# Kernel optimization log

Hardware: AMD Instinct MI355X
Metric: run time of the kernel (lower is better)

Reference implementation:

```python
import jax, jax.numpy as jnp
import numpy as np

B, N, NEMBED, E, H = 4, 256, 10000, 63, 128
D = E + 1  # feature dim after concat = 64


def _lin(key, fan_in, fan_out):
    k1, k2 = jax.random.split(key)
    bound = 1.0 / np.sqrt(fan_in)
    W = jax.random.uniform(k1, (fan_in, fan_out), jnp.float32, -bound, bound)
    b = jax.random.uniform(k2, (fan_out,), jnp.float32, -bound, bound)
    return W, b


def setup_inputs() -> dict:
    key = jax.random.key(0)
    ks = jax.random.split(key, 9)
    xcat = jax.random.randint(ks[0], (B, N), 0, NEMBED, dtype=jnp.int64)
    xfeat = jax.random.normal(ks[1], (B, N), dtype=jnp.float32)
    emb = jax.random.normal(ks[2], (NEMBED, E), dtype=jnp.float32)
    W1, b1 = _lin(ks[3], D, H)
    W2, b2 = _lin(ks[4], H, H)
    W3, b3 = _lin(ks[5], H, H)
    D1, c1 = _lin(ks[6], H, H)
    D2, c2 = _lin(ks[7], H, H)
    D3, c3 = _lin(ks[8], H, 1)
    return {"xcat": xcat, "xfeat": xfeat, "emb": emb,
            "W1": W1, "b1": b1, "W2": W2, "b2": b2, "W3": W3, "b3": b3,
            "D1": D1, "c1": c1, "D2": D2, "c2": c2, "D3": D3, "c3": c3}


def reference(xcat, xfeat, emb, W1, b1, W2, b2, W3, b3, D1, c1, D2, c2, D3, c3):
    # embed + concat scalar feature -> [B, N, D]
    x = jnp.concatenate([emb[xcat], xfeat[..., None]], axis=-1)
    # pairwise outer product over the set dim -> [B, N, N, D]
    # (original: einsum 'bid,bjd->bdij' then permute(0,2,3,1) == 'bid,bjd->bijd')
    p = jnp.einsum('bid,bjd->bijd', x, x)
    # per-pair 3-layer MLP (enc)
    h = jnp.maximum(p @ W1 + b1, 0.0)
    h = jnp.maximum(h @ W2 + b2, 0.0)
    h = h @ W3 + b3
    # relu -> mean pool over (i, j) -> relu; dropout is identity in eval
    h = jnp.maximum(h, 0.0)
    h = jnp.mean(h, axis=(1, 2))  # [B, H]
    h = jnp.maximum(h, 0.0)
    # dec MLP -> [B, 1]
    h = jnp.maximum(h @ D1 + c1, 0.0)
    h = jnp.maximum(h @ D2 + c2, 0.0)
    return h @ D3 + c3
```

## Files before the change

### kernel.cpp

```cpp
#include <hip/hip_runtime.h>
#include <hip/hip_bf16.h>


#define NB 4
#define NN 256
#define HD 128
#define TPB 257

typedef __attribute__((ext_vector_type(8))) short bf16x8;
typedef __attribute__((ext_vector_type(4))) float f32x4;

__device__ __forceinline__ unsigned rne2(float a, float b) {
    unsigned ua = __builtin_bit_cast(unsigned, a);
    unsigned ub = __builtin_bit_cast(unsigned, b);
    ua = ua + 0x7fff + ((ua >> 16) & 1);
    ub = ub + 0x7fff + ((ub >> 16) & 1);
    return (ua >> 16) | (ub & 0xffff0000u);
}

__device__ __forceinline__ short f2bf(float f) {
    unsigned u = __builtin_bit_cast(unsigned, f);
    u = (u + 0x7fff + ((u >> 16) & 1)) >> 16;
    return (short)u;
}

__device__ __forceinline__ void tri_ij(int t, int& i, int& j) {
    j = (int)((sqrtf(8.0f * (float)t + 1.0f) - 1.0f) * 0.5f);
    while (((j + 1) * (j + 2) >> 1) <= t) ++j;
    while (((j * (j + 1)) >> 1) > t) --j;
    i = t - ((j * (j + 1)) >> 1);
}

__device__ __forceinline__ void pack_w(const float* __restrict__ W, short* __restrict__ pw,
                                       int KQ, int u) {
    int l  = u & 63;
    int kq = (u >> 6) % KQ;
    int mt = (u >> 6) / KQ;
    int q = l >> 4, m = l & 15;
    int c = mt * 16 + m;
#pragma unroll
    for (int j = 0; j < 8; ++j) {
        int k = kq * 32 + q * 8 + j;
        pw[u * 8 + j] = f2bf(W[k * 128 + c]);
    }
}

__global__ void prep_kernel(const int* __restrict__ xcat,
                            const float* __restrict__ xfeat,
                            const float* __restrict__ emb,
                            const float* __restrict__ W1,
                            const float* __restrict__ W2,
                            const float* __restrict__ W3,
                            float* __restrict__ x,
                            short* __restrict__ pw1,
                            short* __restrict__ pw2,
                            short* __restrict__ pw3)
{
    int bid = blockIdx.x;
    int tid = threadIdx.x;
    if (bid < 256) {
        int f = bid * 256 + tid;
        int d = f & 63;
        int nn = f >> 6;
        float v;
        if (d < 63) v = emb[xcat[nn] * 63 + d];
        else        v = xfeat[nn];
        x[f] = v;
    } else if (bid < 260) {
        pack_w(W1, pw1, 2, (bid - 256) * 256 + tid);
    } else if (bid < 268) {
        pack_w(W2, pw2, 4, (bid - 260) * 256 + tid);
    } else {
        pack_w(W3, pw3, 4, (bid - 268) * 256 + tid);
    }
}

__global__ __launch_bounds__(256, 3) void pair_mlp(
    const float* __restrict__ x,
    const short* __restrict__ pw1, const float* __restrict__ b1,
    const short* __restrict__ pw2, const float* __restrict__ b2,
    const short* __restrict__ pw3, const float* __restrict__ b3,
    float* __restrict__ partialOut)
{
    __shared__ short smP[128 * 64];
    __shared__ short smH[128 * 128];
    __shared__ float smW[128];

    const int tid = threadIdx.x;
    const int l = tid & 63;
    const int w = __builtin_amdgcn_readfirstlane(tid >> 6);
    const int wm = w >> 1;
    const int wn = w & 1;
    const int q = l >> 4;
    const int m = l & 15;
    const int b = blockIdx.y;
    const int tbase = blockIdx.x * 128;
    const float* xb = x + (b << 14);
    char* smPc = (char*)smP;
    char* smHc = (char*)smH;

    {
        const int p = tid >> 1;
        const int half = tid & 1;
        int i, j;
        tri_ij(tbase + p, i, j);
        if (half == 0) smW[p] = (i == j) ? 1.0f : 2.0f;
        const float4* xi4 = (const float4*)(xb + (i << 6) + half * 32);
        const float4* xj4 = (const float4*)(xb + (j << 6) + half * 32);
#pragma unroll
        for (int c = 0; c < 4; ++c) {
            float4 a0 = xi4[2 * c], a1 = xi4[2 * c + 1];
            float4 u0 = xj4[2 * c], u1 = xj4[2 * c + 1];
            uint4 s;
            s.x = rne2(a0.x * u0.x, a0.y * u0.y);
            s.y = rne2(a0.z * u0.z, a0.w * u0.w);
            s.z = rne2(a1.x * u1.x, a1.y * u1.y);
            s.w = rne2(a1.z * u1.z, a1.w * u1.w);
            int chunk = half * 4 + c;
            int phys = chunk ^ (p & 7);
            *(uint4*)(smPc + p * 128 + phys * 16) = s;
        }
    }
    __syncthreads();

    f32x4 acc[4][4];

#pragma unroll
    for (int mt = 0; mt < 4; ++mt) {
        float4 bv = *(const float4*)(b1 + (wm * 4 + mt) * 16 + q * 4);
        f32x4 init = {bv.x, bv.y, bv.z, bv.w};
#pragma unroll
        for (int nt = 0; nt < 4; ++nt) acc[mt][nt] = init;
    }

#pragma unroll
    for (int kq = 0; kq < 2; ++kq) {
        bf16x8 bfr[4], afr[4];
#pragma unroll
        for (int nt = 0; nt < 4; ++nt) {
            int pair = wn * 64 + nt * 16 + m;
            int phys = (kq * 4 + q) ^ (pair & 7);
            bfr[nt] = *(const bf16x8*)(smPc + pair * 128 + phys * 16);
        }
#pragma unroll
        for (int mt = 0; mt < 4; ++mt)
            afr[mt] = *(const bf16x8*)(pw1 + ((((wm * 4 + mt) * 2 + kq) * 64 + l) << 3));
#pragma unroll
        for (int mt = 0; mt < 4; ++mt)
#pragma unroll
            for (int nt = 0; nt < 4; ++nt)
                acc[mt][nt] = __builtin_amdgcn_mfma_f32_16x16x32_bf16(afr[mt], bfr[nt], acc[mt][nt], 0, 0, 0);
    }

#pragma unroll
    for (int mt = 0; mt < 4; ++mt) {
        int mtg = wm * 4 + mt;
#pragma unroll
        for (int nt = 0; nt < 4; ++nt) {
            int pair = wn * 64 + nt * 16 + m;
            uint2 sv;
            sv.x = rne2(fmaxf(acc[mt][nt][0], 0.f), fmaxf(acc[mt][nt][1], 0.f));
            sv.y = rne2(fmaxf(acc[mt][nt][2], 0.f), fmaxf(acc[mt][nt][3], 0.f));
            int chunk = mtg * 2 + (q >> 1);
            int phys = chunk ^ (pair & 15);
            *(uint2*)(smHc + pair * 256 + phys * 16 + (q & 1) * 8) = sv;
        }
    }
    __syncthreads();

#pragma unroll
    for (int mt = 0; mt < 4; ++mt) {
        float4 bv = *(const float4*)(b2 + (wm * 4 + mt) * 16 + q * 4);
        f32x4 init = {bv.x, bv.y, bv.z, bv.w};
#pragma unroll
        for (int nt = 0; nt < 4; ++nt) acc[mt][nt] = init;
    }

#pragma unroll
    for (int kq = 0; kq < 4; ++kq) {
        bf16x8 bfr[4], afr[4];
#pragma unroll
        for (int nt = 0; nt < 4; ++nt) {
            int pair = wn * 64 + nt * 16 + m;
            int phys = (kq * 4 + q) ^ (pair & 15);
            bfr[nt] = *(const bf16x8*)(smHc + pair * 256 + phys * 16);
        }
#pragma unroll
        for (int mt = 0; mt < 4; ++mt)
            afr[mt] = *(const bf16x8*)(pw2 + ((((wm * 4 + mt) * 4 + kq) * 64 + l) << 3));
#pragma unroll
        for (int mt = 0; mt < 4; ++mt)
#pragma unroll
            for (int nt = 0; nt < 4; ++nt)
                acc[mt][nt] = __builtin_amdgcn_mfma_f32_16x16x32_bf16(afr[mt], bfr[nt], acc[mt][nt], 0, 0, 0);
    }
    __syncthreads();

#pragma unroll
    for (int mt = 0; mt < 4; ++mt) {
        int mtg = wm * 4 + mt;
#pragma unroll
        for (int nt = 0; nt < 4; ++nt) {
            int pair = wn * 64 + nt * 16 + m;
            uint2 sv;
            sv.x = rne2(fmaxf(acc[mt][nt][0], 0.f), fmaxf(acc[mt][nt][1], 0.f));
            sv.y = rne2(fmaxf(acc[mt][nt][2], 0.f), fmaxf(acc[mt][nt][3], 0.f));
            int chunk = mtg * 2 + (q >> 1);
            int phys = chunk ^ (pair & 15);
            *(uint2*)(smHc + pair * 256 + phys * 16 + (q & 1) * 8) = sv;
        }
    }
    __syncthreads();

#pragma unroll
    for (int mt = 0; mt < 4; ++mt) {
        float4 bv = *(const float4*)(b3 + (wm * 4 + mt) * 16 + q * 4);
        f32x4 init = {bv.x, bv.y, bv.z, bv.w};
#pragma unroll
        for (int nt = 0; nt < 4; ++nt) acc[mt][nt] = init;
    }

#pragma unroll
    for (int kq = 0; kq < 4; ++kq) {
        bf16x8 bfr[4], afr[4];
#pragma unroll
        for (int nt = 0; nt < 4; ++nt) {
            int pair = wn * 64 + nt * 16 + m;
            int phys = (kq * 4 + q) ^ (pair & 15);
            bfr[nt] = *(const bf16x8*)(smHc + pair * 256 + phys * 16);
        }
#pragma unroll
        for (int mt = 0; mt < 4; ++mt)
            afr[mt] = *(const bf16x8*)(pw3 + ((((wm * 4 + mt) * 4 + kq) * 64 + l) << 3));
#pragma unroll
        for (int mt = 0; mt < 4; ++mt)
#pragma unroll
            for (int nt = 0; nt < 4; ++nt)
                acc[mt][nt] = __builtin_amdgcn_mfma_f32_16x16x32_bf16(afr[mt], bfr[nt], acc[mt][nt], 0, 0, 0);
    }

    float wpv[4];
#pragma unroll
    for (int nt = 0; nt < 4; ++nt)
        wpv[nt] = smW[wn * 64 + nt * 16 + m];

    float* smPart = (float*)smP;
#pragma unroll
    for (int mt = 0; mt < 4; ++mt) {
        int mtg = wm * 4 + mt;
        float vs[4];
#pragma unroll
        for (int r = 0; r < 4; ++r) {
            vs[r] = wpv[0] * fmaxf(acc[mt][0][r], 0.f) + wpv[1] * fmaxf(acc[mt][1][r], 0.f)
                  + wpv[2] * fmaxf(acc[mt][2][r], 0.f) + wpv[3] * fmaxf(acc[mt][3][r], 0.f);
#pragma unroll
            for (int s = 1; s < 16; s <<= 1)
                vs[r] += __shfl_xor(vs[r], s, 64);
        }
        if (m == 0) {
            float* p = smPart + wn * HD + mtg * 16 + q * 4;
            p[0] = vs[0]; p[1] = vs[1]; p[2] = vs[2]; p[3] = vs[3];
        }
    }
    __syncthreads();

    if (tid < HD) {
        float v = smPart[tid] + smPart[HD + tid];
        partialOut[(b * TPB + blockIdx.x) * HD + tid] = v;
    }
}

__global__ __launch_bounds__(1024) void reduce_decode(
    const float* __restrict__ partial,
    const float* __restrict__ D1, const float* __restrict__ c1,
    const float* __restrict__ D2, const float* __restrict__ c2,
    const float* __restrict__ D3, const float* __restrict__ c3,
    float* __restrict__ out)
{
    __shared__ float red8[8][HD];
    __shared__ float red2[2][HD];
    __shared__ float hb[HD];
    __shared__ float tb[HD];
    const int b = blockIdx.x;
    const int t = threadIdx.x;
    const int ch = t & 127, sl = t >> 7;

    {
        const float* base = partial + b * TPB * HD + ch;
        float s0 = 0.f, s1 = 0.f, s2 = 0.f, s3 = 0.f;
        int tl = sl;
        for (; tl + 32 <= TPB; tl += 32) {
            s0 += base[(tl     ) * HD];
            s1 += base[(tl +  8) * HD];
            s2 += base[(tl + 16) * HD];
            s3 += base[(tl + 24) * HD];
        }
        for (; tl < TPB; tl += 8) s0 += base[tl * HD];
        red8[sl][ch] = (s0 + s1) + (s2 + s3);
    }
    __syncthreads();
    if (sl == 0) {
        float v = ((red8[0][ch] + red8[1][ch]) + (red8[2][ch] + red8[3][ch]))
                + ((red8[4][ch] + red8[5][ch]) + (red8[6][ch] + red8[7][ch]));
        hb[ch] = fmaxf(v * (1.0f / 65536.0f), 0.0f);
    }
    __syncthreads();

    const int hf = sl & 1;

    if (t < 256) {
        float a = 0.f;
        for (int k = hf * 64; k < hf * 64 + 64; ++k)
            a = fmaf(hb[k], D1[(k << 7) + ch], a);
        red2[hf][ch] = a;
    }
    __syncthreads();
    if (t < 128)
        tb[ch] = fmaxf(red2[0][ch] + red2[1][ch] + c1[ch], 0.0f);
    __syncthreads();

    if (t < 256) {
        float a = 0.f;
        for (int k = hf * 64; k < hf * 64 + 64; ++k)
            a = fmaf(tb[k], D2[(k << 7) + ch], a);
        red2[hf][ch] = a;
    }
    __syncthreads();
    if (t < 128)
        hb[ch] = fmaxf(red2[0][ch] + red2[1][ch] + c2[ch], 0.0f);
    __syncthreads();

    if (t < 128) red2[0][ch] = hb[ch] * D3[ch];
    __syncthreads();
    if (t < 64) {
        float r = red2[0][t] + red2[0][t + 64];
#pragma unroll
        for (int s2 = 1; s2 < 64; s2 <<= 1)
            r += __shfl_xor(r, s2, 64);
        if (t == 0) out[b] = r + c3[0];
    }
}

extern "C" void kernel_launch(void* const* d_in, const int* in_sizes, int n_in,
                              void* d_out, int out_size, void* d_ws, size_t ws_size,
                              hipStream_t stream)
{
    (void)in_sizes; (void)n_in; (void)out_size; (void)ws_size;

    const int*   xcat  = (const int*)  d_in[0];
    const float* xfeat = (const float*)d_in[1];
    const float* emb   = (const float*)d_in[2];
    const float* W1    = (const float*)d_in[3];
    const float* b1    = (const float*)d_in[4];
    const float* W2    = (const float*)d_in[5];
    const float* b2    = (const float*)d_in[6];
    const float* W3    = (const float*)d_in[7];
    const float* b3    = (const float*)d_in[8];
    const float* D1    = (const float*)d_in[9];
    const float* c1    = (const float*)d_in[10];
    const float* D2    = (const float*)d_in[11];
    const float* c2    = (const float*)d_in[12];
    const float* D3    = (const float*)d_in[13];
    const float* c3    = (const float*)d_in[14];
    float* out = (float*)d_out;

    float* x       = (float*)d_ws;
    short* pw1     = (short*)(x + NB * NN * 64);
    short* pw2     = pw1 + 8 * 2 * 64 * 8;
    short* pw3     = pw2 + 8 * 4 * 64 * 8;
    float* partial = (float*)(pw3 + 8 * 4 * 64 * 8);

    prep_kernel<<<276, 256, 0, stream>>>(xcat, xfeat, emb, W1, W2, W3,
                                         x, pw1, pw2, pw3);
    pair_mlp<<<dim3(TPB, NB), 256, 0, stream>>>(x, pw1, b1, pw2, b2, pw3, b3, partial);
    reduce_decode<<<NB, 1024, 0, stream>>>(partial, D1, c1, D2, c2, D3, c3, out);
}
```

Measured before the change: 115.9 us.

## Keep inter-layer activations in registers by permuting W2/W3 packing

Each wave now owns 32 pairs and all 128 output channels. The pair products and hidden activations stay in MFMA register fragments instead of passing through shared memory between layers. W2 and W3 are packed with a permuted K order so the accumulator layout of one layer can be reused directly as the B operand of the next. This removes the shared-memory staging and the barriers between layers, but each wave now streams all of the weight fragments from global memory and holds more accumulator registers, which can lower occupancy.

```diff
diff --git a/kernel.cpp b/kernel.cpp
--- a/kernel.cpp
+++ b/kernel.cpp
@@ -31,8 +31,8 @@
     i = t - ((j * (j + 1)) >> 1);
 }
 
-__device__ __forceinline__ void pack_w(const float* __restrict__ W, short* __restrict__ pw,
-                                       int KQ, int u) {
+__device__ __forceinline__ void pack_w_nat(const float* __restrict__ W, short* __restrict__ pw,
+                                           int KQ, int u) {
     int l  = u & 63;
     int kq = (u >> 6) % KQ;
     int mt = (u >> 6) / KQ;
@@ -41,6 +41,20 @@
 #pragma unroll
     for (int j = 0; j < 8; ++j) {
         int k = kq * 32 + q * 8 + j;
+        pw[u * 8 + j] = f2bf(W[k * 128 + c]);
+    }
+}
+
+__device__ __forceinline__ void pack_w_perm(const float* __restrict__ W, short* __restrict__ pw,
+                                            int u) {
+    int l  = u & 63;
+    int kq = (u >> 6) & 3;
+    int mt = (u >> 6) >> 2;
+    int q = l >> 4, m = l & 15;
+    int c = mt * 16 + m;
+#pragma unroll
+    for (int j = 0; j < 8; ++j) {
+        int k = 32 * kq + 16 * (j >> 2) + 4 * q + (j & 3);
         pw[u * 8 + j] = f2bf(W[k * 128 + c]);
     }
 }
@@ -67,11 +81,11 @@
         else        v = xfeat[nn];
         x[f] = v;
     } else if (bid < 260) {
-        pack_w(W1, pw1, 2, (bid - 256) * 256 + tid);
+        pack_w_nat(W1, pw1, 2, (bid - 256) * 256 + tid);
     } else if (bid < 268) {
-        pack_w(W2, pw2, 4, (bid - 260) * 256 + tid);
+        pack_w_perm(W2, pw2, (bid - 260) * 256 + tid);
     } else {
-        pack_w(W3, pw3, 4, (bid - 268) * 256 + tid);
+        pack_w_perm(W3, pw3, (bid - 268) * 256 + tid);
     }
 }
 
@@ -82,190 +96,140 @@
     const short* __restrict__ pw3, const float* __restrict__ b3,
     float* __restrict__ partialOut)
 {
-    __shared__ short smP[128 * 64];
-    __shared__ short smH[128 * 128];
-    __shared__ float smW[128];
+    __shared__ float smPart[4][HD];
 
     const int tid = threadIdx.x;
+    const int w = __builtin_amdgcn_readfirstlane(tid >> 6);
     const int l = tid & 63;
-    const int w = __builtin_amdgcn_readfirstlane(tid >> 6);
-    const int wm = w >> 1;
-    const int wn = w & 1;
     const int q = l >> 4;
-    const int m = l & 15;
+    const int n = l & 15;
     const int b = blockIdx.y;
-    const int tbase = blockIdx.x * 128;
     const float* xb = x + (b << 14);
-    char* smPc = (char*)smP;
-    char* smHc = (char*)smH;
-
+
+    const int p0 = blockIdx.x * 128 + w * 32 + n;
+    int i0, j0, i1, j1;
+    tri_ij(p0, i0, j0);
+    tri_ij(p0 + 16, i1, j1);
+    const float wp0 = (i0 == j0) ? 1.0f : 2.0f;
+    const float wp1 = (i1 == j1) ? 1.0f : 2.0f;
+
+    bf16x8 bp[2][2];
     {
-        const int p = tid >> 1;
-        const int half = tid & 1;
-        int i, j;
-        tri_ij(tbase + p, i, j);
-        if (half == 0) smW[p] = (i == j) ? 1.0f : 2.0f;
-        const float4* xi4 = (const float4*)(xb + (i << 6) + half * 32);
-        const float4* xj4 = (const float4*)(xb + (j << 6) + half * 32);
-#pragma unroll
-        for (int c = 0; c < 4; ++c) {
-            float4 a0 = xi4[2 * c], a1 = xi4[2 * c + 1];
-            float4 u0 = xj4[2 * c], u1 = xj4[2 * c + 1];
-            uint4 s;
-            s.x = rne2(a0.x * u0.x, a0.y * u0.y);
-            s.y = rne2(a0.z * u0.z, a0.w * u0.w);
-            s.z = rne2(a1.x * u1.x, a1.y * u1.y);
-            s.w = rne2(a1.z * u1.z, a1.w * u1.w);
-            int chunk = half * 4 + c;
-            int phys = chunk ^ (p & 7);
-            *(uint4*)(smPc + p * 128 + phys * 16) = s;
-        }
-    }
-    __syncthreads();
-
-    f32x4 acc[4][4];
-
-#pragma unroll
-    for (int mt = 0; mt < 4; ++mt) {
-        float4 bv = *(const float4*)(b1 + (wm * 4 + mt) * 16 + q * 4);
+        const float* xi[2] = {xb + (i0 << 6), xb + (i1 << 6)};
+        const float* xj[2] = {xb + (j0 << 6), xb + (j1 << 6)};
+#pragma unroll
+        for (int nt = 0; nt < 2; ++nt)
+#pragma unroll
+            for (int kq = 0; kq < 2; ++kq) {
+                int dd = kq * 32 + q * 8;
+                float4 A0 = *(const float4*)(xi[nt] + dd);
+                float4 A1 = *(const float4*)(xi[nt] + dd + 4);
+                float4 B0 = *(const float4*)(xj[nt] + dd);
+                float4 B1 = *(const float4*)(xj[nt] + dd + 4);
+                uint4 s;
+                s.x = rne2(A0.x * B0.x, A0.y * B0.y);
+                s.y = rne2(A0.z * B0.z, A0.w * B0.w);
+                s.z = rne2(A1.x * B1.x, A1.y * B1.y);
+                s.w = rne2(A1.z * B1.z, A1.w * B1.w);
+                bp[nt][kq] = __builtin_bit_cast(bf16x8, s);
+            }
+    }
+
+    f32x4 acc[8][2];
+    unsigned pk[2][8][2];
+
+#pragma unroll
+    for (int mt = 0; mt < 8; ++mt) {
+        float4 bv = *(const float4*)(b1 + mt * 16 + q * 4);
         f32x4 init = {bv.x, bv.y, bv.z, bv.w};
-#pragma unroll
-        for (int nt = 0; nt < 4; ++nt) acc[mt][nt] = init;
-    }
-
-#pragma unroll
-    for (int kq = 0; kq < 2; ++kq) {
-        bf16x8 bfr[4], afr[4];
-#pragma unroll
-        for (int nt = 0; nt < 4; ++nt) {
-            int pair = wn * 64 + nt * 16 + m;
-            int phys = (kq * 4 + q) ^ (pair & 7);
-            bfr[nt] = *(const bf16x8*)(smPc + pair * 128 + phys * 16);
-        }
-#pragma unroll
-        for (int mt = 0; mt < 4; ++mt)
-            afr[mt] = *(const bf16x8*)(pw1 + ((((wm * 4 + mt) * 2 + kq) * 64 + l) << 3));
-#pragma unroll
-        for (int mt = 0; mt < 4; ++mt)
-#pragma unroll
-            for (int nt = 0; nt < 4; ++nt)
-                acc[mt][nt] = __builtin_amdgcn_mfma_f32_16x16x32_bf16(afr[mt], bfr[nt], acc[mt][nt], 0, 0, 0);
-    }
-
-#pragma unroll
-    for (int mt = 0; mt < 4; ++mt) {
-        int mtg = wm * 4 + mt;
-#pragma unroll
-        for (int nt = 0; nt < 4; ++nt) {
-            int pair = wn * 64 + nt * 16 + m;
-            uint2 sv;
-            sv.x = rne2(fmaxf(acc[mt][nt][0], 0.f), fmaxf(acc[mt][nt][1], 0.f));
-            sv.y = rne2(fmaxf(acc[mt][nt][2], 0.f), fmaxf(acc[mt][nt][3], 0.f));
-            int chunk = mtg * 2 + (q >> 1);
-            int phys = chunk ^ (pair & 15);
-            *(uint2*)(smHc + pair * 256 + phys * 16 + (q & 1) * 8) = sv;
-        }
-    }
-    __syncthreads();
-
-#pragma unroll
-    for (int mt = 0; mt < 4; ++mt) {
-        float4 bv = *(const float4*)(b2 + (wm * 4 + mt) * 16 + q * 4);
+        acc[mt][0] = init; acc[mt][1] = init;
+    }
+#pragma unroll
+    for (int kq = 0; kq < 2; ++kq)
+#pragma unroll
+        for (int mt = 0; mt < 8; ++mt) {
+            bf16x8 afr = *(const bf16x8*)(pw1 + (((mt * 2 + kq) * 64 + l) << 3));
+            acc[mt][0] = __builtin_amdgcn_mfma_f32_16x16x32_bf16(afr, bp[0][kq], acc[mt][0], 0, 0, 0);
+            acc[mt][1] = __builtin_amdgcn_mfma_f32_16x16x32_bf16(afr, bp[1][kq], acc[mt][1], 0, 0, 0);
+        }
+
+#pragma unroll
+    for (int nt = 0; nt < 2; ++nt)
+#pragma unroll
+        for (int mt = 0; mt < 8; ++mt) {
+            pk[nt][mt][0] = rne2(fmaxf(acc[mt][nt][0], 0.f), fmaxf(acc[mt][nt][1], 0.f));
+            pk[nt][mt][1] = rne2(fmaxf(acc[mt][nt][2], 0.f), fmaxf(acc[mt][nt][3], 0.f));
+        }
+
+#pragma unroll
+    for (int mt = 0; mt < 8; ++mt) {
+        float4 bv = *(const float4*)(b2 + mt * 16 + q * 4);
         f32x4 init = {bv.x, bv.y, bv.z, bv.w};
-#pragma unroll
-        for (int nt = 0; nt < 4; ++nt) acc[mt][nt] = init;
-    }
-
+        acc[mt][0] = init; acc[mt][1] = init;
+    }
 #pragma unroll
     for (int kq = 0; kq < 4; ++kq) {
-        bf16x8 bfr[4], afr[4];
-#pragma unroll
-        for (int nt = 0; nt < 4; ++nt) {
-            int pair = wn * 64 + nt * 16 + m;
-            int phys = (kq * 4 + q) ^ (pair & 15);
-            bfr[nt] = *(const bf16x8*)(smHc + pair * 256 + phys * 16);
-        }
-#pragma unroll
-        for (int mt = 0; mt < 4; ++mt)
-            afr[mt] = *(const bf16x8*)(pw2 + ((((wm * 4 + mt) * 4 + kq) * 64 + l) << 3));
-#pragma unroll
-        for (int mt = 0; mt < 4; ++mt)
-#pragma unroll
-            for (int nt = 0; nt < 4; ++nt)
-                acc[mt][nt] = __builtin_amdgcn_mfma_f32_16x16x32_bf16(afr[mt], bfr[nt], acc[mt][nt], 0, 0, 0);
-    }
-    __syncthreads();
-
-#pragma unroll
-    for (int mt = 0; mt < 4; ++mt) {
-        int mtg = wm * 4 + mt;
-#pragma unroll
-        for (int nt = 0; nt < 4; ++nt) {
-            int pair = wn * 64 + nt * 16 + m;
-            uint2 sv;
-            sv.x = rne2(fmaxf(acc[mt][nt][0], 0.f), fmaxf(acc[mt][nt][1], 0.f));
-            sv.y = rne2(fmaxf(acc[mt][nt][2], 0.f), fmaxf(acc[mt][nt][3], 0.f));
-            int chunk = mtg * 2 + (q >> 1);
-            int phys = chunk ^ (pair & 15);
-            *(uint2*)(smHc + pair * 256 + phys * 16 + (q & 1) * 8) = sv;
-        }
-    }
-    __syncthreads();
-
-#pragma unroll
-    for (int mt = 0; mt < 4; ++mt) {
-        float4 bv = *(const float4*)(b3 + (wm * 4 + mt) * 16 + q * 4);
+        uint4 u0 = {pk[0][2 * kq][0], pk[0][2 * kq][1], pk[0][2 * kq + 1][0], pk[0][2 * kq + 1][1]};
+        uint4 u1 = {pk[1][2 * kq][0], pk[1][2 * kq][1], pk[1][2 * kq + 1][0], pk[1][2 * kq + 1][1]};
+        bf16x8 bf0 = __builtin_bit_cast(bf16x8, u0);
+        bf16x8 bf1 = __builtin_bit_cast(bf16x8, u1);
+#pragma unroll
+        for (int mt = 0; mt < 8; ++mt) {
+            bf16x8 afr = *(const bf16x8*)(pw2 + (((mt * 4 + kq) * 64 + l) << 3));
+            acc[mt][0] = __builtin_amdgcn_mfma_f32_16x16x32_bf16(afr, bf0, acc[mt][0], 0, 0, 0);
+            acc[mt][1] = __builtin_amdgcn_mfma_f32_16x16x32_bf16(afr, bf1, acc[mt][1], 0, 0, 0);
+        }
+    }
+
+#pragma unroll
+    for (int nt = 0; nt < 2; ++nt)
+#pragma unroll
+        for (int mt = 0; mt < 8; ++mt) {
+            pk[nt][mt][0] = rne2(fmaxf(acc[mt][nt][0], 0.f), fmaxf(acc[mt][nt][1], 0.f));
+            pk[nt][mt][1] = rne2(fmaxf(acc[mt][nt][2], 0.f), fmaxf(acc[mt][nt][3], 0.f));
+        }
+
+#pragma unroll
+    for (int mt = 0; mt < 8; ++mt) {
+        float4 bv = *(const float4*)(b3 + mt * 16 + q * 4);
         f32x4 init = {bv.x, bv.y, bv.z, bv.w};
-#pragma unroll
-        for (int nt = 0; nt < 4; ++nt) acc[mt][nt] = init;
-    }
-
+        acc[mt][0] = init; acc[mt][1] = init;
+    }
 #pragma unroll
     for (int kq = 0; kq < 4; ++kq) {
-        bf16x8 bfr[4], afr[4];
-#pragma unroll
-        for (int nt = 0; nt < 4; ++nt) {
-            int pair = wn * 64 + nt * 16 + m;
-            int phys = (kq * 4 + q) ^ (pair & 15);
-            bfr[nt] = *(const bf16x8*)(smHc + pair * 256 + phys * 16);
-        }
-#pragma unroll
-        for (int mt = 0; mt < 4; ++mt)
-            afr[mt] = *(const bf16x8*)(pw3 + ((((wm * 4 + mt) * 4 + kq) * 64 + l) << 3));
-#pragma unroll
-        for (int mt = 0; mt < 4; ++mt)
-#pragma unroll
-            for (int nt = 0; nt < 4; ++nt)
-                acc[mt][nt] = __builtin_amdgcn_mfma_f32_16x16x32_bf16(afr[mt], bfr[nt], acc[mt][nt], 0, 0, 0);
-    }
-
-    float wpv[4];
-#pragma unroll
-    for (int nt = 0; nt < 4; ++nt)
-        wpv[nt] = smW[wn * 64 + nt * 16 + m];
-
-    float* smPart = (float*)smP;
-#pragma unroll
-    for (int mt = 0; mt < 4; ++mt) {
-        int mtg = wm * 4 + mt;
+        uint4 u0 = {pk[0][2 * kq][0], pk[0][2 * kq][1], pk[0][2 * kq + 1][0], pk[0][2 * kq + 1][1]};
+        uint4 u1 = {pk[1][2 * kq][0], pk[1][2 * kq][1], pk[1][2 * kq + 1][0], pk[1][2 * kq + 1][1]};
+        bf16x8 bf0 = __builtin_bit_cast(bf16x8, u0);
+        bf16x8 bf1 = __builtin_bit_cast(bf16x8, u1);
+#pragma unroll
+        for (int mt = 0; mt < 8; ++mt) {
+            bf16x8 afr = *(const bf16x8*)(pw3 + (((mt * 4 + kq) * 64 + l) << 3));
+            acc[mt][0] = __builtin_amdgcn_mfma_f32_16x16x32_bf16(afr, bf0, acc[mt][0], 0, 0, 0);
+            acc[mt][1] = __builtin_amdgcn_mfma_f32_16x16x32_bf16(afr, bf1, acc[mt][1], 0, 0, 0);
+        }
+    }
+
+#pragma unroll
+    for (int mt = 0; mt < 8; ++mt) {
         float vs[4];
 #pragma unroll
         for (int r = 0; r < 4; ++r) {
-            vs[r] = wpv[0] * fmaxf(acc[mt][0][r], 0.f) + wpv[1] * fmaxf(acc[mt][1][r], 0.f)
-                  + wpv[2] * fmaxf(acc[mt][2][r], 0.f) + wpv[3] * fmaxf(acc[mt][3][r], 0.f);
-#pragma unroll
-            for (int s = 1; s < 16; s <<= 1)
-                vs[r] += __shfl_xor(vs[r], s, 64);
-        }
-        if (m == 0) {
-            float* p = smPart + wn * HD + mtg * 16 + q * 4;
-            p[0] = vs[0]; p[1] = vs[1]; p[2] = vs[2]; p[3] = vs[3];
+            float v = wp0 * fmaxf(acc[mt][0][r], 0.f) + wp1 * fmaxf(acc[mt][1][r], 0.f);
+            v += __shfl_xor(v, 1, 64);
+            v += __shfl_xor(v, 2, 64);
+            v += __shfl_xor(v, 4, 64);
+            v += __shfl_xor(v, 8, 64);
+            vs[r] = v;
+        }
+        if (n == 0) {
+            float4 o = {vs[0], vs[1], vs[2], vs[3]};
+            *(float4*)(&smPart[w][mt * 16 + q * 4]) = o;
         }
     }
     __syncthreads();
 
     if (tid < HD) {
-        float v = smPart[tid] + smPart[HD + tid];
+        float v = (smPart[0][tid] + smPart[1][tid]) + (smPart[2][tid] + smPart[3][tid]);
         partialOut[(b * TPB + blockIdx.x) * HD + tid] = v;
     }
 }
```

New measurement: 131.4 us. +13.4%, slower.

## Build pair-product fragments directly in registers, dropping the smP staging buffer

Applied to the files above, without the earlier changes.

The outer-product B fragments for layer 1 are now computed per lane from global x loads straight into MFMA registers, removing the shared-memory staging tile, its barrier and the smW weight table. Pair weights are computed in registers. The freed LDS lets occupancy rise to 4 blocks per CU via launch bounds, and the partial-sum scratch now reuses smH after an added barrier. In exchange, each wave does more redundant global/L1 loads of x rows (each element loaded by several waves), and the higher occupancy target may increase register pressure.

```diff
diff --git a/kernel.cpp b/kernel.cpp
--- a/kernel.cpp
+++ b/kernel.cpp
@@ -75,16 +75,14 @@
     }
 }
 
-__global__ __launch_bounds__(256, 3) void pair_mlp(
+__global__ __launch_bounds__(256, 4) void pair_mlp(
     const float* __restrict__ x,
     const short* __restrict__ pw1, const float* __restrict__ b1,
     const short* __restrict__ pw2, const float* __restrict__ b2,
     const short* __restrict__ pw3, const float* __restrict__ b3,
     float* __restrict__ partialOut)
 {
-    __shared__ short smP[128 * 64];
     __shared__ short smH[128 * 128];
-    __shared__ float smW[128];
 
     const int tid = threadIdx.x;
     const int l = tid & 63;
@@ -96,32 +94,16 @@
     const int b = blockIdx.y;
     const int tbase = blockIdx.x * 128;
     const float* xb = x + (b << 14);
-    char* smPc = (char*)smP;
     char* smHc = (char*)smH;
 
-    {
-        const int p = tid >> 1;
-        const int half = tid & 1;
-        int i, j;
-        tri_ij(tbase + p, i, j);
-        if (half == 0) smW[p] = (i == j) ? 1.0f : 2.0f;
-        const float4* xi4 = (const float4*)(xb + (i << 6) + half * 32);
-        const float4* xj4 = (const float4*)(xb + (j << 6) + half * 32);
-#pragma unroll
-        for (int c = 0; c < 4; ++c) {
-            float4 a0 = xi4[2 * c], a1 = xi4[2 * c + 1];
-            float4 u0 = xj4[2 * c], u1 = xj4[2 * c + 1];
-            uint4 s;
-            s.x = rne2(a0.x * u0.x, a0.y * u0.y);
-            s.y = rne2(a0.z * u0.z, a0.w * u0.w);
-            s.z = rne2(a1.x * u1.x, a1.y * u1.y);
-            s.w = rne2(a1.z * u1.z, a1.w * u1.w);
-            int chunk = half * 4 + c;
-            int phys = chunk ^ (p & 7);
-            *(uint4*)(smPc + p * 128 + phys * 16) = s;
-        }
-    }
-    __syncthreads();
+    int iv[4], jv[4];
+    float wpv[4];
+#pragma unroll
+    for (int nt = 0; nt < 4; ++nt) {
+        int p = tbase + wn * 64 + nt * 16 + m;
+        tri_ij(p, iv[nt], jv[nt]);
+        wpv[nt] = (iv[nt] == jv[nt]) ? 1.0f : 2.0f;
+    }
 
     f32x4 acc[4][4];
 
@@ -136,11 +118,21 @@
 #pragma unroll
     for (int kq = 0; kq < 2; ++kq) {
         bf16x8 bfr[4], afr[4];
-#pragma unroll
-        for (int nt = 0; nt < 4; ++nt) {
-            int pair = wn * 64 + nt * 16 + m;
-            int phys = (kq * 4 + q) ^ (pair & 7);
-            bfr[nt] = *(const bf16x8*)(smPc + pair * 128 + phys * 16);
+        const int dd = kq * 32 + q * 8;
+#pragma unroll
+        for (int nt = 0; nt < 4; ++nt) {
+            const float* xi = xb + (iv[nt] << 6) + dd;
+            const float* xj = xb + (jv[nt] << 6) + dd;
+            float4 A0 = *(const float4*)(xi);
+            float4 A1 = *(const float4*)(xi + 4);
+            float4 B0 = *(const float4*)(xj);
+            float4 B1 = *(const float4*)(xj + 4);
+            uint4 s;
+            s.x = rne2(A0.x * B0.x, A0.y * B0.y);
+            s.y = rne2(A0.z * B0.z, A0.w * B0.w);
+            s.z = rne2(A1.x * B1.x, A1.y * B1.y);
+            s.w = rne2(A1.z * B1.z, A1.w * B1.w);
+            bfr[nt] = __builtin_bit_cast(bf16x8, s);
         }
 #pragma unroll
         for (int mt = 0; mt < 4; ++mt)
@@ -238,13 +230,9 @@
             for (int nt = 0; nt < 4; ++nt)
                 acc[mt][nt] = __builtin_amdgcn_mfma_f32_16x16x32_bf16(afr[mt], bfr[nt], acc[mt][nt], 0, 0, 0);
     }
-
-    float wpv[4];
-#pragma unroll
-    for (int nt = 0; nt < 4; ++nt)
-        wpv[nt] = smW[wn * 64 + nt * 16 + m];
-
-    float* smPart = (float*)smP;
+    __syncthreads();
+
+    float* smPart = (float*)smH;
 #pragma unroll
     for (int mt = 0; mt < 4; ++mt) {
         int mtg = wm * 4 + mt;
```

Result: slower. 130.6 us (+12.7%).
